# Kernel optimization log

Hardware: AMD Instinct MI355X
Metric: run time of the kernel (lower is better)

The kernel has to match this reference:

```python
import jax, jax.numpy as jnp
import numpy as np

EMB = 1024
NH = 16
HS = EMB // NH  # 64


def setup_inputs() -> dict:
    key = jax.random.key(0)
    k_x, k_wqkv, k_bqkv, k_wo, k_bo = jax.random.split(key, 5)
    x = jax.random.normal(k_x, (4, 2048, EMB), dtype=jnp.float32)
    s = 1.0 / np.sqrt(EMB)
    # torch nn.Linear weight is [out, in]; store as [in, out] for x @ W
    w_qkv = jax.random.uniform(k_wqkv, (EMB, 3 * EMB), dtype=jnp.float32, minval=-s, maxval=s)
    b_qkv = jax.random.uniform(k_bqkv, (3 * EMB,), dtype=jnp.float32, minval=-s, maxval=s)
    w_out = jax.random.uniform(k_wo, (EMB, EMB), dtype=jnp.float32, minval=-s, maxval=s)
    b_out = jax.random.uniform(k_bo, (EMB,), dtype=jnp.float32, minval=-s, maxval=s)
    return {"x": x, "w_qkv": w_qkv, "b_qkv": b_qkv, "w_out": w_out, "b_out": b_out}


def reference(x, w_qkv, b_qkv, w_out, b_out):
    B, T, C = x.shape
    qkv = x @ w_qkv + b_qkv  # [B, T, 3*C]
    q, k, v = jnp.split(qkv, 3, axis=-1)
    # [B, T, C] -> [B, nh, T, hs]
    def heads(t):
        return t.reshape(B, T, NH, HS).transpose(0, 2, 1, 3)
    q, k, v = heads(q), heads(k), heads(v)
    scores = jnp.einsum('bhqd,bhkd->bhqk', q, k) / jnp.sqrt(jnp.float32(HS))
    attn = jax.nn.softmax(scores, axis=-1)  # dropout=0 -> identity
    out = jnp.einsum('bhqk,bhkd->bhqd', attn, v)
    out = out.transpose(0, 2, 1, 3).reshape(B, T, NH * HS)
    return out @ w_out + b_out
```

## Files before the change

### kernel.cpp

```cpp
#include <hip/hip_runtime.h>

typedef unsigned short u16;
typedef unsigned int u32;
typedef __attribute__((ext_vector_type(8))) __bf16 bf16x8;
typedef __attribute__((ext_vector_type(4))) __bf16 bf16x4;
typedef __attribute__((ext_vector_type(4))) float f32x4;

#define GLD_AS1 const __attribute__((address_space(1))) void*
#define GLD_AS3 __attribute__((address_space(3))) void*

__device__ __forceinline__ u16 f2b(float f) {
  u32 u = __builtin_bit_cast(u32, f);
  u += 0x7fffu + ((u >> 16) & 1u);
  return (u16)(u >> 16);
}

__global__ void cvt_x_kernel(const float* __restrict__ in, u16* __restrict__ out, int n) {
  int i4 = (blockIdx.x * blockDim.x + threadIdx.x) * 4;
  if (i4 < n) {
    float4 v = *(const float4*)(in + i4);
    ushort4 o;
    o.x = f2b(v.x); o.y = f2b(v.y); o.z = f2b(v.z); o.w = f2b(v.w);
    *(ushort4*)(out + i4) = o;
  }
}

__global__ void transpose_w_kernel(const float* __restrict__ src, u16* __restrict__ dst,
                                   int R, int C) {
  __shared__ float tile[32][33];
  int c0 = blockIdx.x * 32, r0 = blockIdx.y * 32;
  int tx = threadIdx.x & 31, ty = threadIdx.x >> 5;
  #pragma unroll
  for (int i = ty; i < 32; i += 8)
    tile[i][tx] = src[(size_t)(r0 + i) * C + c0 + tx];
  __syncthreads();
  #pragma unroll
  for (int i = ty; i < 32; i += 8)
    dst[(size_t)(c0 + i) * R + r0 + tx] = f2b(tile[tx][i]);
}

__global__ void transpose_v_kernel(const u16* __restrict__ v, u16* __restrict__ vt) {
  __shared__ u16 tile[64][68];
  int t0 = blockIdx.x * 64;
  int bh = blockIdx.y;
  int tx = threadIdx.x & 31, ty = threadIdx.x >> 5;
  const u16* src = v + (size_t)bh * 2048 * 64;
  u16* dst = vt + (size_t)bh * 64 * 2048;
  #pragma unroll
  for (int i = ty; i < 64; i += 8)
    *(u32*)&tile[i][tx * 2] = *(const u32*)&src[(size_t)(t0 + i) * 64 + tx * 2];
  __syncthreads();
  const int c = tx * 2;
  const int e = c & 3, g = (c >> 2) & 3, hi = (c >> 4) & 1;
  const int cp = (c & 32) | (8 * g + 4 * hi + e);
  #pragma unroll
  for (int d = ty; d < 64; d += 8) {
    u32 a = tile[c][d];
    u32 b = tile[c + 1][d];
    *(u32*)&dst[(size_t)d * 2048 + t0 + cp] = a | (b << 16);
  }
}

template <int MODE>
__global__ __launch_bounds__(256)
void gemm_kernel(const u16* __restrict__ A, const u16* __restrict__ Bt,
                 const float* __restrict__ bias,
                 u16* __restrict__ qo, u16* __restrict__ ko, u16* __restrict__ vo,
                 float* __restrict__ outF, int N, int K) {
  __shared__ u16 As[128 * 64];
  __shared__ u16 Bs[128 * 64];
  const int tid = threadIdx.x;
  const int lane = tid & 63, wave = tid >> 6;
  const int m0 = blockIdx.x * 128, n0 = blockIdx.y * 128;
  const int wm = (wave >> 1) * 64, wn = (wave & 1) * 64;
  const int lr = lane & 15, lg = lane >> 4;

  const int rA = tid >> 3;
  const int kbs = ((tid & 7) * 16) ^ ((rA & 7) << 4);

  const char* Ab = (const char*)(A + (size_t)m0 * K);
  const char* Bb = (const char*)(Bt + (size_t)n0 * K);
  const size_t strideB = (size_t)K * 2;

  f32x4 acc[4][4] = {};
  const int swr = (lr & 7) << 4;

  const int nk = K >> 6;
  for (int kt = 0; kt < nk; ++kt) {
    const int kb0 = kt * 128;
    #pragma unroll
    for (int i = 0; i < 4; ++i)
      __builtin_amdgcn_global_load_lds(
          (GLD_AS1)(Ab + (size_t)(i * 32 + rA) * strideB + kb0 + kbs),
          (GLD_AS3)((char*)As + i * 4096 + tid * 16), 16, 0, 0);
    #pragma unroll
    for (int i = 0; i < 4; ++i)
      __builtin_amdgcn_global_load_lds(
          (GLD_AS1)(Bb + (size_t)(i * 32 + rA) * strideB + kb0 + kbs),
          (GLD_AS3)((char*)Bs + i * 4096 + tid * 16), 16, 0, 0);
    __syncthreads();

    bf16x8 af[4][2], bfr[4][2];
    #pragma unroll
    for (int m = 0; m < 4; ++m) {
      int row = wm + m * 16 + lr;
      #pragma unroll
      for (int s = 0; s < 2; ++s)
        af[m][s] = *(const bf16x8*)((const char*)As + row * 128 + ((s * 64 + lg * 16) ^ swr));
    }
    #pragma unroll
    for (int n = 0; n < 4; ++n) {
      int row = wn + n * 16 + lr;
      #pragma unroll
      for (int s = 0; s < 2; ++s)
        bfr[n][s] = *(const bf16x8*)((const char*)Bs + row * 128 + ((s * 64 + lg * 16) ^ swr));
    }
    #pragma unroll
    for (int m = 0; m < 4; ++m)
      #pragma unroll
      for (int n = 0; n < 4; ++n) {
        acc[m][n] = __builtin_amdgcn_mfma_f32_16x16x32_bf16(af[m][0], bfr[n][0], acc[m][n], 0, 0, 0);
        acc[m][n] = __builtin_amdgcn_mfma_f32_16x16x32_bf16(af[m][1], bfr[n][1], acc[m][n], 0, 0, 0);
      }
    __syncthreads();
  }

  #pragma unroll
  for (int n = 0; n < 4; ++n) {
    const int col = n0 + wn + n * 16 + lr;
    const float bv = bias[col];
    #pragma unroll
    for (int m = 0; m < 4; ++m) {
      const int rowb = m0 + wm + m * 16 + lg * 4;
      #pragma unroll
      for (int j = 0; j < 4; ++j) {
        float val = acc[m][n][j] + bv;
        int row = rowb + j;
        if (MODE == 0) {
          int which = col >> 10, c = col & 1023;
          int h = c >> 6, d = c & 63;
          int b = row >> 11, t = row & 2047;
          if (which == 0) val *= 0.18033688011112042f;
          u16* dst = which == 0 ? qo : (which == 1 ? ko : vo);
          dst[((size_t)(b * 16 + h) * 2048 + t) * 64 + d] = f2b(val);
        } else {
          outF[(size_t)row * N + col] = val;
        }
      }
    }
  }
}

__global__ __launch_bounds__(512)
void attn_kernel(const u16* __restrict__ Q, const u16* __restrict__ Kg,
                 const u16* __restrict__ Vt, u16* __restrict__ att) {
  const int tid = threadIdx.x;
  const int wave = tid >> 6, lane = tid & 63;
  const int lr = lane & 15, lg = lane >> 4;
  const int bh = blockIdx.x;
  const int q0 = blockIdx.y * 256;
  const int b = bh >> 4, h = bh & 15;

  const u16* Qh = Q + (size_t)bh * 2048 * 64;
  const char* Khb = (const char*)(Kg + (size_t)bh * 2048 * 64);
  const char* Vhb = (const char*)(Vt + (size_t)bh * 64 * 2048);

  __shared__ u16 Ks[3][64 * 64];
  __shared__ u16 Vs[3][64 * 64];

  const int rS = tid >> 3;
  const int cS = ((tid & 7) * 16) ^ ((rS & 7) << 4);

  bf16x8 qf[2][2];
  #pragma unroll
  for (int m = 0; m < 2; ++m)
    #pragma unroll
    for (int s = 0; s < 2; ++s)
      qf[m][s] = *(const bf16x8*)(Qh + (size_t)(q0 + wave * 32 + m * 16 + lr) * 64 + s * 32 + lg * 8);

  bf16x8 ones;
  #pragma unroll
  for (int e = 0; e < 8; ++e) ones[e] = (__bf16)1.0f;

  f32x4 acc[2][4] = {};
  f32x4 accl[2] = {};

#define STAGE(T, BUF)                                                          \
  {                                                                            \
    __builtin_amdgcn_global_load_lds(                                          \
        (GLD_AS1)(Khb + (size_t)((T) * 64 + rS) * 128 + cS),                   \
        (GLD_AS3)((char*)Ks[BUF] + tid * 16), 16, 0, 0);                       \
    __builtin_amdgcn_global_load_lds(                                          \
        (GLD_AS1)(Vhb + (size_t)rS * 4096 + (T) * 128 + cS),                   \
        (GLD_AS3)((char*)Vs[BUF] + tid * 16), 16, 0, 0);                       \
  }

  STAGE(0, 0);
  STAGE(1, 1);

  for (int kt = 0; kt < 32; ++kt) {
    if (kt == 31) { asm volatile("s_waitcnt vmcnt(0)" ::: "memory"); }
    else          { asm volatile("s_waitcnt vmcnt(2)" ::: "memory"); }
    __builtin_amdgcn_sched_barrier(0);
    __builtin_amdgcn_s_barrier();
    if (kt < 30) STAGE(kt + 2, (kt + 2) % 3);
    const int cur = kt % 3;

    #pragma unroll
    for (int ks = 0; ks < 2; ++ks) {
      f32x4 sf0[2] = {}, sf1[2] = {};
      __builtin_amdgcn_s_setprio(1);
      #pragma unroll
      for (int s = 0; s < 2; ++s) {
        bf16x8 kf0 = *(const bf16x8*)((const char*)Ks[cur] + (2 * ks * 16 + lr) * 128 +
                                      ((s * 64 + lg * 16) ^ ((lr & 7) << 4)));
        sf0[0] = __builtin_amdgcn_mfma_f32_16x16x32_bf16(kf0, qf[0][s], sf0[0], 0, 0, 0);
        sf0[1] = __builtin_amdgcn_mfma_f32_16x16x32_bf16(kf0, qf[1][s], sf0[1], 0, 0, 0);
        bf16x8 kf1 = *(const bf16x8*)((const char*)Ks[cur] + ((2 * ks + 1) * 16 + lr) * 128 +
                                      ((s * 64 + lg * 16) ^ ((lr & 7) << 4)));
        sf1[0] = __builtin_amdgcn_mfma_f32_16x16x32_bf16(kf1, qf[0][s], sf1[0], 0, 0, 0);
        sf1[1] = __builtin_amdgcn_mfma_f32_16x16x32_bf16(kf1, qf[1][s], sf1[1], 0, 0, 0);
      }
      __builtin_amdgcn_s_setprio(0);

      bf16x8 pa[2];
      #pragma unroll
      for (int m = 0; m < 2; ++m)
        #pragma unroll
        for (int j = 0; j < 4; ++j) {
          pa[m][j]     = (__bf16)__builtin_amdgcn_exp2f(sf0[m][j]);
          pa[m][4 + j] = (__bf16)__builtin_amdgcn_exp2f(sf1[m][j]);
        }

      __builtin_amdgcn_s_setprio(1);
      accl[0] = __builtin_amdgcn_mfma_f32_16x16x32_bf16(ones, pa[0], accl[0], 0, 0, 0);
      accl[1] = __builtin_amdgcn_mfma_f32_16x16x32_bf16(ones, pa[1], accl[1], 0, 0, 0);
      #pragma unroll
      for (int d = 0; d < 4; ++d) {
        const int rv = d * 16 + lr;
        bf16x8 vf = *(const bf16x8*)((const char*)Vs[cur] + rv * 128 +
                                     ((64 * ks + 16 * lg) ^ ((lr & 7) << 4)));
        acc[0][d] = __builtin_amdgcn_mfma_f32_16x16x32_bf16(vf, pa[0], acc[0][d], 0, 0, 0);
        acc[1][d] = __builtin_amdgcn_mfma_f32_16x16x32_bf16(vf, pa[1], acc[1][d], 0, 0, 0);
      }
      __builtin_amdgcn_s_setprio(0);
    }
  }

  #pragma unroll
  for (int m = 0; m < 2; ++m) {
    const float inv = 1.0f / accl[m][0];
    const int t = q0 + wave * 32 + m * 16 + lr;
    #pragma unroll
    for (int d = 0; d < 4; ++d) {
      bf16x4 ov;
      #pragma unroll
      for (int j = 0; j < 4; ++j) ov[j] = (__bf16)(acc[m][d][j] * inv);
      *(bf16x4*)&att[((size_t)b * 2048 + t) * 1024 + h * 64 + d * 16 + lg * 4] = ov;
    }
  }
#undef STAGE
}

extern "C" void kernel_launch(void* const* d_in, const int* in_sizes, int n_in,
                              void* d_out, int out_size, void* d_ws, size_t ws_size,
                              hipStream_t stream) {
  const float* x     = (const float*)d_in[0];
  const float* w_qkv = (const float*)d_in[1];
  const float* b_qkv = (const float*)d_in[2];
  const float* w_out = (const float*)d_in[3];
  const float* b_out = (const float*)d_in[4];
  float* out = (float*)d_out;

  char* ws = (char*)d_ws;
  const size_t MB = 1024 * 1024;
  u16* xb    = (u16*)(ws);
  u16* wqkvt = (u16*)(ws + 16 * MB);
  u16* woutt = (u16*)(ws + 22 * MB);
  u16* qb    = (u16*)(ws + 24 * MB);
  u16* kb    = (u16*)(ws + 40 * MB);
  u16* vb    = (u16*)(ws + 56 * MB);
  u16* vtb   = (u16*)(ws + 72 * MB);
  u16* attb  = xb;

  {
    int n = 4 * 2048 * 1024;
    cvt_x_kernel<<<(n / 4 + 255) / 256, 256, 0, stream>>>(x, xb, n);
  }
  transpose_w_kernel<<<dim3(3072 / 32, 1024 / 32), 256, 0, stream>>>(w_qkv, wqkvt, 1024, 3072);
  transpose_w_kernel<<<dim3(1024 / 32, 1024 / 32), 256, 0, stream>>>(w_out, woutt, 1024, 1024);

  gemm_kernel<0><<<dim3(8192 / 128, 3072 / 128), 256, 0, stream>>>(
      xb, wqkvt, b_qkv, qb, kb, vb, nullptr, 3072, 1024);

  transpose_v_kernel<<<dim3(2048 / 64, 64), 256, 0, stream>>>(vb, vtb);

  attn_kernel<<<dim3(64, 8), 512, 0, stream>>>(qb, kb, vtb, attb);

  gemm_kernel<1><<<dim3(8192 / 128, 1024 / 128), 256, 0, stream>>>(
      attb, woutt, b_out, nullptr, nullptr, nullptr, out, 1024, 1024);
}
```

Before: 184.7 us.

## Triple-buffer GEMM LDS tiles with async prefetch and enlarge block to 256x128

```diff
diff --git a/kernel.cpp b/kernel.cpp
--- a/kernel.cpp
+++ b/kernel.cpp
@@ -62,43 +62,54 @@
 }
 
 template <int MODE>
-__global__ __launch_bounds__(256)
+__global__ __launch_bounds__(512, 2)
 void gemm_kernel(const u16* __restrict__ A, const u16* __restrict__ Bt,
                  const float* __restrict__ bias,
                  u16* __restrict__ qo, u16* __restrict__ ko, u16* __restrict__ vo,
                  float* __restrict__ outF, int N, int K) {
-  __shared__ u16 As[128 * 64];
-  __shared__ u16 Bs[128 * 64];
+  __shared__ u16 As[3][256 * 64];
+  __shared__ u16 Bs[3][128 * 64];
   const int tid = threadIdx.x;
   const int lane = tid & 63, wave = tid >> 6;
-  const int m0 = blockIdx.x * 128, n0 = blockIdx.y * 128;
+  const int m0 = blockIdx.x * 256, n0 = blockIdx.y * 128;
   const int wm = (wave >> 1) * 64, wn = (wave & 1) * 64;
   const int lr = lane & 15, lg = lane >> 4;
 
   const int rA = tid >> 3;
-  const int kbs = ((tid & 7) * 16) ^ ((rA & 7) << 4);
+  const int cSw = ((tid & 7) * 16) ^ ((rA & 7) << 4);
 
   const char* Ab = (const char*)(A + (size_t)m0 * K);
   const char* Bb = (const char*)(Bt + (size_t)n0 * K);
-  const size_t strideB = (size_t)K * 2;
+  const size_t strideK = (size_t)K * 2;
 
   f32x4 acc[4][4] = {};
   const int swr = (lr & 7) << 4;
 
+#define GSTAGE(T, BUF)                                                         \
+  {                                                                            \
+    _Pragma("unroll")                                                          \
+    for (int i = 0; i < 4; ++i)                                                \
+      __builtin_amdgcn_global_load_lds(                                        \
+          (GLD_AS1)(Ab + (size_t)(i * 64 + rA) * strideK + (T) * 128 + cSw),   \
+          (GLD_AS3)((char*)As[BUF] + i * 8192 + tid * 16), 16, 0, 0);          \
+    _Pragma("unroll")                                                          \
+    for (int i = 0; i < 2; ++i)                                                \
+      __builtin_amdgcn_global_load_lds(                                        \
+          (GLD_AS1)(Bb + (size_t)(i * 64 + rA) * strideK + (T) * 128 + cSw),   \
+          (GLD_AS3)((char*)Bs[BUF] + i * 8192 + tid * 16), 16, 0, 0);          \
+  }
+
   const int nk = K >> 6;
+  GSTAGE(0, 0);
+  GSTAGE(1, 1);
+
   for (int kt = 0; kt < nk; ++kt) {
-    const int kb0 = kt * 128;
-    #pragma unroll
-    for (int i = 0; i < 4; ++i)
-      __builtin_amdgcn_global_load_lds(
-          (GLD_AS1)(Ab + (size_t)(i * 32 + rA) * strideB + kb0 + kbs),
-          (GLD_AS3)((char*)As + i * 4096 + tid * 16), 16, 0, 0);
-    #pragma unroll
-    for (int i = 0; i < 4; ++i)
-      __builtin_amdgcn_global_load_lds(
-          (GLD_AS1)(Bb + (size_t)(i * 32 + rA) * strideB + kb0 + kbs),
-          (GLD_AS3)((char*)Bs + i * 4096 + tid * 16), 16, 0, 0);
-    __syncthreads();
+    if (kt == nk - 1) { asm volatile("s_waitcnt vmcnt(0)" ::: "memory"); }
+    else              { asm volatile("s_waitcnt vmcnt(6)" ::: "memory"); }
+    __builtin_amdgcn_sched_barrier(0);
+    __builtin_amdgcn_s_barrier();
+    if (kt < nk - 2) GSTAGE(kt + 2, (kt + 2) % 3);
+    const int cur = kt % 3;
 
     bf16x8 af[4][2], bfr[4][2];
     #pragma unroll
@@ -106,15 +117,16 @@
       int row = wm + m * 16 + lr;
       #pragma unroll
       for (int s = 0; s < 2; ++s)
-        af[m][s] = *(const bf16x8*)((const char*)As + row * 128 + ((s * 64 + lg * 16) ^ swr));
+        af[m][s] = *(const bf16x8*)((const char*)As[cur] + row * 128 + ((s * 64 + lg * 16) ^ swr));
     }
     #pragma unroll
     for (int n = 0; n < 4; ++n) {
       int row = wn + n * 16 + lr;
       #pragma unroll
       for (int s = 0; s < 2; ++s)
-        bfr[n][s] = *(const bf16x8*)((const char*)Bs + row * 128 + ((s * 64 + lg * 16) ^ swr));
-    }
+        bfr[n][s] = *(const bf16x8*)((const char*)Bs[cur] + row * 128 + ((s * 64 + lg * 16) ^ swr));
+    }
+    __builtin_amdgcn_s_setprio(1);
     #pragma unroll
     for (int m = 0; m < 4; ++m)
       #pragma unroll
@@ -122,8 +134,9 @@
         acc[m][n] = __builtin_amdgcn_mfma_f32_16x16x32_bf16(af[m][0], bfr[n][0], acc[m][n], 0, 0, 0);
         acc[m][n] = __builtin_amdgcn_mfma_f32_16x16x32_bf16(af[m][1], bfr[n][1], acc[m][n], 0, 0, 0);
       }
-    __syncthreads();
-  }
+    __builtin_amdgcn_s_setprio(0);
+  }
+#undef GSTAGE
 
   #pragma unroll
   for (int n = 0; n < 4; ++n) {
@@ -290,13 +303,13 @@
   transpose_w_kernel<<<dim3(3072 / 32, 1024 / 32), 256, 0, stream>>>(w_qkv, wqkvt, 1024, 3072);
   transpose_w_kernel<<<dim3(1024 / 32, 1024 / 32), 256, 0, stream>>>(w_out, woutt, 1024, 1024);
 
-  gemm_kernel<0><<<dim3(8192 / 128, 3072 / 128), 256, 0, stream>>>(
+  gemm_kernel<0><<<dim3(8192 / 256, 3072 / 128), 512, 0, stream>>>(
       xb, wqkvt, b_qkv, qb, kb, vb, nullptr, 3072, 1024);
 
   transpose_v_kernel<<<dim3(2048 / 64, 64), 256, 0, stream>>>(vb, vtb);
 
   attn_kernel<<<dim3(64, 8), 512, 0, stream>>>(qb, kb, vtb, attb);
 
-  gemm_kernel<1><<<dim3(8192 / 128, 1024 / 128), 256, 0, stream>>>(
+  gemm_kernel<1><<<dim3(8192 / 256, 1024 / 128), 512, 0, stream>>>(
       attb, woutt, b_out, nullptr, nullptr, nullptr, out, 1024, 1024);
 }
```

Result: no change. 187.6 us (+1.6%).

## Fuse fp32-to-bf16 conversion of x into the QKV GEMM A-tile load

Applied to the files above, without the earlier changes.

```diff
diff --git a/kernel.cpp b/kernel.cpp
--- a/kernel.cpp
+++ b/kernel.cpp
@@ -13,16 +13,6 @@
   u32 u = __builtin_bit_cast(u32, f);
   u += 0x7fffu + ((u >> 16) & 1u);
   return (u16)(u >> 16);
-}
-
-__global__ void cvt_x_kernel(const float* __restrict__ in, u16* __restrict__ out, int n) {
-  int i4 = (blockIdx.x * blockDim.x + threadIdx.x) * 4;
-  if (i4 < n) {
-    float4 v = *(const float4*)(in + i4);
-    ushort4 o;
-    o.x = f2b(v.x); o.y = f2b(v.y); o.z = f2b(v.z); o.w = f2b(v.w);
-    *(ushort4*)(out + i4) = o;
-  }
 }
 
 __global__ void transpose_w_kernel(const float* __restrict__ src, u16* __restrict__ dst,
@@ -63,58 +53,79 @@
 
 template <int MODE>
 __global__ __launch_bounds__(256)
-void gemm_kernel(const u16* __restrict__ A, const u16* __restrict__ Bt,
+void gemm_kernel(const void* __restrict__ Ap, const u16* __restrict__ Bt,
                  const float* __restrict__ bias,
                  u16* __restrict__ qo, u16* __restrict__ ko, u16* __restrict__ vo,
                  float* __restrict__ outF, int N, int K) {
-  __shared__ u16 As[128 * 64];
-  __shared__ u16 Bs[128 * 64];
+  __shared__ char As[(MODE == 0) ? 32768 : 16384];
+  __shared__ char Bs[16384];
   const int tid = threadIdx.x;
   const int lane = tid & 63, wave = tid >> 6;
   const int m0 = blockIdx.x * 128, n0 = blockIdx.y * 128;
   const int wm = (wave >> 1) * 64, wn = (wave & 1) * 64;
   const int lr = lane & 15, lg = lane >> 4;
 
-  const int rA = tid >> 3;
-  const int kbs = ((tid & 7) * 16) ^ ((rA & 7) << 4);
-
-  const char* Ab = (const char*)(A + (size_t)m0 * K);
+  const int rB = tid >> 3;
+  const int cB = ((tid & 7) * 16) ^ ((rB & 7) << 4);
+  const int rA16 = tid >> 4;
+  const int cA = ((tid & 15) * 16) ^ (rA16 << 4);
+
+  const size_t strideA = (size_t)K * (MODE == 0 ? 4 : 2);
+  const size_t strideB = (size_t)K * 2;
+  const char* Ab = (const char*)Ap + (size_t)m0 * strideA;
   const char* Bb = (const char*)(Bt + (size_t)n0 * K);
-  const size_t strideB = (size_t)K * 2;
 
   f32x4 acc[4][4] = {};
   const int swr = (lr & 7) << 4;
 
   const int nk = K >> 6;
   for (int kt = 0; kt < nk; ++kt) {
-    const int kb0 = kt * 128;
+    if (MODE == 0) {
+      #pragma unroll
+      for (int i = 0; i < 8; ++i)
+        __builtin_amdgcn_global_load_lds(
+            (GLD_AS1)(Ab + (size_t)(i * 16 + rA16) * strideA + kt * 256 + cA),
+            (GLD_AS3)(As + i * 4096 + tid * 16), 16, 0, 0);
+    } else {
+      #pragma unroll
+      for (int i = 0; i < 4; ++i)
+        __builtin_amdgcn_global_load_lds(
+            (GLD_AS1)(Ab + (size_t)(i * 32 + rB) * strideA + kt * 128 + cB),
+            (GLD_AS3)(As + i * 4096 + tid * 16), 16, 0, 0);
+    }
     #pragma unroll
     for (int i = 0; i < 4; ++i)
       __builtin_amdgcn_global_load_lds(
-          (GLD_AS1)(Ab + (size_t)(i * 32 + rA) * strideB + kb0 + kbs),
-          (GLD_AS3)((char*)As + i * 4096 + tid * 16), 16, 0, 0);
-    #pragma unroll
-    for (int i = 0; i < 4; ++i)
-      __builtin_amdgcn_global_load_lds(
-          (GLD_AS1)(Bb + (size_t)(i * 32 + rA) * strideB + kb0 + kbs),
-          (GLD_AS3)((char*)Bs + i * 4096 + tid * 16), 16, 0, 0);
+          (GLD_AS1)(Bb + (size_t)(i * 32 + rB) * strideB + kt * 128 + cB),
+          (GLD_AS3)(Bs + i * 4096 + tid * 16), 16, 0, 0);
     __syncthreads();
 
     bf16x8 af[4][2], bfr[4][2];
     #pragma unroll
     for (int m = 0; m < 4; ++m) {
-      int row = wm + m * 16 + lr;
+      const int row = wm + m * 16 + lr;
+      #pragma unroll
+      for (int s = 0; s < 2; ++s) {
+        if (MODE == 0) {
+          f32x4 a0 = *(const f32x4*)(As + row * 256 + ((s * 128 + lg * 32) ^ (lr << 4)));
+          f32x4 a1 = *(const f32x4*)(As + row * 256 + ((s * 128 + lg * 32 + 16) ^ (lr << 4)));
+          bf16x8 v;
+          #pragma unroll
+          for (int e = 0; e < 4; ++e) { v[e] = (__bf16)a0[e]; v[4 + e] = (__bf16)a1[e]; }
+          af[m][s] = v;
+        } else {
+          af[m][s] = *(const bf16x8*)(As + row * 128 + ((s * 64 + lg * 16) ^ swr));
+        }
+      }
+    }
+    #pragma unroll
+    for (int n = 0; n < 4; ++n) {
+      const int row = wn + n * 16 + lr;
       #pragma unroll
       for (int s = 0; s < 2; ++s)
-        af[m][s] = *(const bf16x8*)((const char*)As + row * 128 + ((s * 64 + lg * 16) ^ swr));
-    }
-    #pragma unroll
-    for (int n = 0; n < 4; ++n) {
-      int row = wn + n * 16 + lr;
-      #pragma unroll
-      for (int s = 0; s < 2; ++s)
-        bfr[n][s] = *(const bf16x8*)((const char*)Bs + row * 128 + ((s * 64 + lg * 16) ^ swr));
-    }
+        bfr[n][s] = *(const bf16x8*)(Bs + row * 128 + ((s * 64 + lg * 16) ^ swr));
+    }
+    __builtin_amdgcn_s_setprio(1);
     #pragma unroll
     for (int m = 0; m < 4; ++m)
       #pragma unroll
@@ -122,6 +133,7 @@
         acc[m][n] = __builtin_amdgcn_mfma_f32_16x16x32_bf16(af[m][0], bfr[n][0], acc[m][n], 0, 0, 0);
         acc[m][n] = __builtin_amdgcn_mfma_f32_16x16x32_bf16(af[m][1], bfr[n][1], acc[m][n], 0, 0, 0);
       }
+    __builtin_amdgcn_s_setprio(0);
     __syncthreads();
   }
 
@@ -274,24 +286,19 @@
 
   char* ws = (char*)d_ws;
   const size_t MB = 1024 * 1024;
-  u16* xb    = (u16*)(ws);
+  u16* attb  = (u16*)(ws);
   u16* wqkvt = (u16*)(ws + 16 * MB);
   u16* woutt = (u16*)(ws + 22 * MB);
   u16* qb    = (u16*)(ws + 24 * MB);
   u16* kb    = (u16*)(ws + 40 * MB);
   u16* vb    = (u16*)(ws + 56 * MB);
   u16* vtb   = (u16*)(ws + 72 * MB);
-  u16* attb  = xb;
-
-  {
-    int n = 4 * 2048 * 1024;
-    cvt_x_kernel<<<(n / 4 + 255) / 256, 256, 0, stream>>>(x, xb, n);
-  }
+
   transpose_w_kernel<<<dim3(3072 / 32, 1024 / 32), 256, 0, stream>>>(w_qkv, wqkvt, 1024, 3072);
   transpose_w_kernel<<<dim3(1024 / 32, 1024 / 32), 256, 0, stream>>>(w_out, woutt, 1024, 1024);
 
   gemm_kernel<0><<<dim3(8192 / 128, 3072 / 128), 256, 0, stream>>>(
-      xb, wqkvt, b_qkv, qb, kb, vb, nullptr, 3072, 1024);
+      x, wqkvt, b_qkv, qb, kb, vb, nullptr, 3072, 1024);
 
   transpose_v_kernel<<<dim3(2048 / 64, 64), 256, 0, stream>>>(vb, vtb);
 
```

After: 183.8 us. About the same (-0.5%).
